# Kernel tuning notes

Measured on AMD Instinct MI355X. Metric: run time of the kernel, lower is better.

The kernel has to match this reference:

```python
import jax, jax.numpy as jnp
import numpy as np

H = 16       # attention heads
DH = 128     # head dim (H*DH = hidden)

def layer_norm(x, scale, bias, eps=1e-5):
    mu = jnp.mean(x, axis=-1, keepdims=True)
    var = jnp.mean(jnp.square(x - mu), axis=-1, keepdims=True)
    return (x - mu) * jax.lax.rsqrt(var + eps) * scale + bias

def transformer_layer(x, ln1_scale, ln1_bias, wq, wk, wv, wo, ln2_scale, ln2_bias, w_ff1, w_ff2):
    B, S, D = x.shape
    xn = layer_norm(x, ln1_scale, ln1_bias)
    q = (xn @ wq.T).reshape(B, S, H, DH)
    k = (xn @ wk.T).reshape(B, S, H, DH)
    v = (xn @ wv.T).reshape(B, S, H, DH)
    scores = jnp.einsum('bqhd,bkhd->bhqk', q, k) / np.sqrt(DH).astype(np.float32)
    causal = jnp.tril(jnp.ones((S, S), dtype=bool))
    scores = jnp.where(causal, scores, jnp.float32(-1e9))
    attn = jax.nn.softmax(scores, axis=-1)
    ctx = jnp.einsum('bhqk,bkhd->bqhd', attn, v).reshape(B, S, D)
    x = x + ctx @ wo.T
    xn2 = layer_norm(x, ln2_scale, ln2_bias)
    x = x + jax.nn.gelu(xn2 @ w_ff1.T) @ w_ff2.T
    return x

def setup_inputs() -> dict:
    key = jax.random.key(0)
    ks = jax.random.split(key, 16)
    B, S, D, R, F = 2, 2048, 2048, 32, 8192
    sd = 1.0 / np.sqrt(D)
    inp = {
        'hidden_states': jax.random.normal(ks[0], (B, S, D), jnp.float32),
        'simple_bias': jnp.zeros((D,), jnp.float32),
        'w_down': jax.random.normal(ks[1], (R, D), jnp.float32) * (0.1 * np.sqrt(2.0 / (D + R))),
        'w_up': jax.random.normal(ks[2], (D, R), jnp.float32) * (0.1 * np.sqrt(2.0 / (D + R))),
        'w_router': jax.random.normal(ks[3], (3, D), jnp.float32) * sd,
        'ln1_scale': jnp.ones((D,), jnp.float32),
        'ln1_bias': jnp.zeros((D,), jnp.float32),
        'wq': jax.random.normal(ks[4], (D, D), jnp.float32) * sd,
        'wk': jax.random.normal(ks[5], (D, D), jnp.float32) * sd,
        'wv': jax.random.normal(ks[6], (D, D), jnp.float32) * sd,
        'wo': jax.random.normal(ks[7], (D, D), jnp.float32) * sd,
        'ln2_scale': jnp.ones((D,), jnp.float32),
        'ln2_bias': jnp.zeros((D,), jnp.float32),
        'w_ff1': jax.random.normal(ks[8], (F, D), jnp.float32) * sd,
        'w_ff2': jax.random.normal(ks[9], (D, F), jnp.float32) * (1.0 / np.sqrt(F)),
    }
    return inp

def reference(hidden_states, simple_bias, w_down, w_up, w_router,
              ln1_scale, ln1_bias, wq, wk, wv, wo,
              ln2_scale, ln2_bias, w_ff1, w_ff2):
    # Router: per-token logits over 3 paths, hard argmax decision
    route_logits = hidden_states @ w_router.T           # [B,S,3]
    route_decisions = jnp.argmax(route_logits, axis=-1)  # [B,S] int
    # Path 0: simple bias add
    out0 = hidden_states + simple_bias
    # Path 1: low-rank residual adapter
    out1 = hidden_states + (hidden_states @ w_down.T) @ w_up.T
    # Path 2: full transformer layer
    out2 = transformer_layer(hidden_states, ln1_scale, ln1_bias, wq, wk, wv, wo,
                             ln2_scale, ln2_bias, w_ff1, w_ff2)
    d = route_decisions[..., None]
    output = jnp.where(d == 0, out0, jnp.where(d == 1, out1, out2))
    return output
```

## Files before the change

### kernel.cpp

```cpp
#include <hip/hip_runtime.h>
#include <math.h>

#define Tn 4096
#define Dn 2048
#define Sn 2048
#define Hn 16
#define Fn 8192
#define Rn 32
#define FC 2048

typedef short bf16x8 __attribute__((ext_vector_type(8)));
typedef float f32x4 __attribute__((ext_vector_type(4)));

union U8 { unsigned short s[8]; uint4 v; };

__device__ __forceinline__ float gelu_f(float x) {
  return 0.5f * x * (1.0f + tanhf(0.7978845608028654f * (x + 0.044715f * x * x * x)));
}

__device__ __forceinline__ unsigned short f2bf(float x) {
  union { float f; unsigned u; } v; v.f = x;
  unsigned r = v.u + 0x7FFFu + ((v.u >> 16) & 1u);
  return (unsigned short)(r >> 16);
}
__device__ __forceinline__ float bf2f(unsigned short h) {
  union { unsigned u; float f; } v; v.u = ((unsigned)h) << 16; return v.f;
}

__device__ __forceinline__ void glds16(const unsigned short* g, unsigned short* lds) {
  __builtin_amdgcn_global_load_lds((const __attribute__((address_space(1))) void*)g,
                                   (__attribute__((address_space(3))) void*)lds, 16, 0, 0);
}

__global__ __launch_bounds__(256)
void ln_router_kernel(const float* __restrict__ x,
                      const float* __restrict__ sc,
                      const float* __restrict__ bi,
                      const float* __restrict__ wr,
                      unsigned short* __restrict__ xh,
                      unsigned short* __restrict__ xl,
                      int* __restrict__ dec)
{
  const int t = blockIdx.x;
  const int tid = threadIdx.x;
  const float* row = x + (size_t)t * Dn;
  const int d0 = tid * 8;
  float4 v0 = *(const float4*)(row + d0);
  float4 v1 = *(const float4*)(row + d0 + 4);
  float a[5];
  a[0] = v0.x + v0.y + v0.z + v0.w + v1.x + v1.y + v1.z + v1.w;
  a[1] = v0.x*v0.x + v0.y*v0.y + v0.z*v0.z + v0.w*v0.w
       + v1.x*v1.x + v1.y*v1.y + v1.z*v1.z + v1.w*v1.w;
  a[2] = 0.f; a[3] = 0.f; a[4] = 0.f;
  if (wr) {
#pragma unroll
    for (int r = 0; r < 3; ++r) {
      float4 w0 = *(const float4*)(wr + r * Dn + d0);
      float4 w1 = *(const float4*)(wr + r * Dn + d0 + 4);
      a[2 + r] = v0.x*w0.x + v0.y*w0.y + v0.z*w0.z + v0.w*w0.w
               + v1.x*w1.x + v1.y*w1.y + v1.z*w1.z + v1.w*w1.w;
    }
  }
#pragma unroll
  for (int i = 0; i < 5; ++i) {
#pragma unroll
    for (int off = 32; off > 0; off >>= 1)
      a[i] += __shfl_down(a[i], off);
  }
  __shared__ float red[4][5];
  __shared__ float fin[5];
  const int wv = tid >> 6, ln = tid & 63;
  if (ln == 0) {
#pragma unroll
    for (int i = 0; i < 5; ++i) red[wv][i] = a[i];
  }
  __syncthreads();
  if (tid == 0) {
#pragma unroll
    for (int i = 0; i < 5; ++i)
      fin[i] = red[0][i] + red[1][i] + red[2][i] + red[3][i];
    if (dec) {
      float l0 = fin[2], l1 = fin[3], l2 = fin[4];
      int best = 0; float bl = l0;
      if (l1 > bl) { best = 1; bl = l1; }
      if (l2 > bl) { best = 2; }
      dec[t] = best;
    }
  }
  __syncthreads();
  const float mu  = fin[0] * (1.0f / Dn);
  const float var = fin[1] * (1.0f / Dn) - mu * mu;
  const float rs  = rsqrtf(var + 1e-5f);
  float4 s0 = *(const float4*)(sc + d0);
  float4 s1 = *(const float4*)(sc + d0 + 4);
  float4 b0 = *(const float4*)(bi + d0);
  float4 b1 = *(const float4*)(bi + d0 + 4);
  float o[8];
  o[0] = (v0.x - mu) * rs * s0.x + b0.x;
  o[1] = (v0.y - mu) * rs * s0.y + b0.y;
  o[2] = (v0.z - mu) * rs * s0.z + b0.z;
  o[3] = (v0.w - mu) * rs * s0.w + b0.w;
  o[4] = (v1.x - mu) * rs * s1.x + b1.x;
  o[5] = (v1.y - mu) * rs * s1.y + b1.y;
  o[6] = (v1.z - mu) * rs * s1.z + b1.z;
  o[7] = (v1.w - mu) * rs * s1.w + b1.w;
  U8 hu, lu;
#pragma unroll
  for (int j = 0; j < 8; ++j) {
    hu.s[j] = f2bf(o[j]);
    lu.s[j] = f2bf(o[j] - bf2f(hu.s[j]));
  }
  *(uint4*)&xh[(size_t)t * Dn + d0] = hu.v;
  *(uint4*)&xl[(size_t)t * Dn + d0] = lu.v;
}

__global__ __launch_bounds__(256)
void cvt_pair_kernel(const float* __restrict__ src, int ld, int K,
                     unsigned short* __restrict__ H, unsigned short* __restrict__ L,
                     int total8)
{
  int i = blockIdx.x * 256 + threadIdx.x;
  if (i >= total8) return;
  size_t e = (size_t)i * 8;
  int row = (int)(e / (size_t)K);
  int col = (int)(e % (size_t)K);
  const float* s = src + (size_t)row * ld + col;
  float4 v0 = *(const float4*)s;
  float4 v1 = *(const float4*)(s + 4);
  float o[8] = {v0.x, v0.y, v0.z, v0.w, v1.x, v1.y, v1.z, v1.w};
  U8 hu, lu;
#pragma unroll
  for (int j = 0; j < 8; ++j) {
    hu.s[j] = f2bf(o[j]);
    lu.s[j] = f2bf(o[j] - bf2f(hu.s[j]));
  }
  *(uint4*)&H[e] = hu.v;
  *(uint4*)&L[e] = lu.v;
}

#define BM 128
#define BN 128
#define BK 32
__global__ __launch_bounds__(256)
void gemm_bf16s(const unsigned short* __restrict__ Ah, const unsigned short* __restrict__ Al,
                const unsigned short* __restrict__ Bh, const unsigned short* __restrict__ Bl,
                int K, float* __restrict__ C, const float* __restrict__ resid,
                unsigned short* __restrict__ Gh, unsigned short* __restrict__ Gl,
                int N, int mode)
{
  __shared__ unsigned short sAh[BM * BK];
  __shared__ unsigned short sAl[BM * BK];
  __shared__ unsigned short sBh[BN * BK];
  __shared__ unsigned short sBl[BN * BK];
  const int tid = threadIdx.x;
  const int l = tid & 63, w = tid >> 6;
  const int wm = w >> 1, wn = w & 1;
  const int fr = l & 15, kg = (l >> 4) * 8;
  const int bm = blockIdx.y * BM, bn = blockIdx.x * BN;

  f32x4 acc[4][4];
#pragma unroll
  for (int m = 0; m < 4; ++m)
#pragma unroll
    for (int n = 0; n < 4; ++n)
#pragma unroll
      for (int q = 0; q < 4; ++q) acc[m][n][q] = 0.f;

  for (int k0 = 0; k0 < K; k0 += BK) {
#pragma unroll
    for (int r = 0; r < 2; ++r) {
      const int c = r * 256 + tid;
      const int row = c >> 2, q = c & 3;
      const size_t ga = (size_t)(bm + row) * K + k0 + q * 8;
      const size_t gb = (size_t)(bn + row) * K + k0 + q * 8;
      const int ub = (r * 256 + w * 64) * 8;
      glds16(Ah + ga, sAh + ub);
      glds16(Al + ga, sAl + ub);
      glds16(Bh + gb, sBh + ub);
      glds16(Bl + gb, sBl + ub);
    }
    __syncthreads();

    bf16x8 ah[4], al[4], bh[4], bl[4];
#pragma unroll
    for (int m = 0; m < 4; ++m) {
      const int ro = (wm * 64 + m * 16 + fr) * BK + kg;
      ah[m] = *(const bf16x8*)&sAh[ro];
      al[m] = *(const bf16x8*)&sAl[ro];
    }
#pragma unroll
    for (int n = 0; n < 4; ++n) {
      const int ro = (wn * 64 + n * 16 + fr) * BK + kg;
      bh[n] = *(const bf16x8*)&sBh[ro];
      bl[n] = *(const bf16x8*)&sBl[ro];
    }
#pragma unroll
    for (int m = 0; m < 4; ++m)
#pragma unroll
      for (int n = 0; n < 4; ++n) {
        acc[m][n] = __builtin_amdgcn_mfma_f32_16x16x32_bf16(ah[m], bh[n], acc[m][n], 0, 0, 0);
        acc[m][n] = __builtin_amdgcn_mfma_f32_16x16x32_bf16(ah[m], bl[n], acc[m][n], 0, 0, 0);
        acc[m][n] = __builtin_amdgcn_mfma_f32_16x16x32_bf16(al[m], bh[n], acc[m][n], 0, 0, 0);
      }
    __syncthreads();
  }

  const int rbase = (l >> 4) * 4;
#pragma unroll
  for (int m = 0; m < 4; ++m) {
#pragma unroll
    for (int i = 0; i < 4; ++i) {
      const int row = bm + wm * 64 + m * 16 + rbase + i;
#pragma unroll
      for (int n = 0; n < 4; ++n) {
        const int col = bn + wn * 64 + n * 16 + fr;
        float v = acc[m][n][i];
        const size_t idx = (size_t)row * N + col;
        if (mode & 5) {
          float g = (mode & 1) ? gelu_f(v) : v;
          unsigned short h = f2bf(g);
          Gh[idx] = h;
          Gl[idx] = f2bf(g - bf2f(h));
        } else {
          if (resid) v += resid[idx];
          if (mode & 2) v += C[idx];
          C[idx] = v;
        }
      }
    }
  }
}

#define GBM 128
#define GBN 128
#define GBK 16
__global__ __launch_bounds__(256)
void gemm_nt(const float* __restrict__ A, int lda,
             const float* __restrict__ B, int ldb,
             float* __restrict__ C, int ldc,
             const float* __restrict__ resid,
             int M, int N, int K, int flags)
{
  __shared__ float As[GBK][GBM + 4];
  __shared__ float Bs[GBK][GBN + 4];
  const int bm = blockIdx.y * GBM;
  const int bn = blockIdx.x * GBN;
  const int tid = threadIdx.x;
  const int ty = tid >> 4, tx = tid & 15;
  float acc[8][8];
#pragma unroll
  for (int i = 0; i < 8; ++i)
#pragma unroll
    for (int j = 0; j < 8; ++j) acc[i][j] = 0.f;

  for (int k0 = 0; k0 < K; k0 += GBK) {
#pragma unroll
    for (int i = 0; i < 2; ++i) {
      int fid = tid + i * 256;
      int row = fid >> 2, c = (fid & 3) << 2;
      float4 av = *(const float4*)(A + (size_t)(bm + row) * lda + k0 + c);
      As[c + 0][row] = av.x; As[c + 1][row] = av.y;
      As[c + 2][row] = av.z; As[c + 3][row] = av.w;
      float4 bv = make_float4(0.f, 0.f, 0.f, 0.f);
      if (bn + row < N)
        bv = *(const float4*)(B + (size_t)(bn + row) * ldb + k0 + c);
      Bs[c + 0][row] = bv.x; Bs[c + 1][row] = bv.y;
      Bs[c + 2][row] = bv.z; Bs[c + 3][row] = bv.w;
    }
    __syncthreads();
#pragma unroll
    for (int k = 0; k < GBK; ++k) {
      float4 a0 = *(const float4*)&As[k][ty * 4];
      float4 a1 = *(const float4*)&As[k][64 + ty * 4];
      float4 b0 = *(const float4*)&Bs[k][tx * 4];
      float4 b1 = *(const float4*)&Bs[k][64 + tx * 4];
      float aa[8] = {a0.x, a0.y, a0.z, a0.w, a1.x, a1.y, a1.z, a1.w};
      float bb[8] = {b0.x, b0.y, b0.z, b0.w, b1.x, b1.y, b1.z, b1.w};
#pragma unroll
      for (int i = 0; i < 8; ++i)
#pragma unroll
        for (int j = 0; j < 8; ++j)
          acc[i][j] += aa[i] * bb[j];
    }
    __syncthreads();
  }
#pragma unroll
  for (int i = 0; i < 8; ++i) {
    int row = bm + ((i < 4) ? (ty * 4 + i) : (64 + ty * 4 + i - 4));
#pragma unroll
    for (int jj = 0; jj < 2; ++jj) {
      int col = bn + ((jj == 0) ? (tx * 4) : (64 + tx * 4));
      if (col < N) {
        float4 o;
        o.x = acc[i][jj * 4 + 0]; o.y = acc[i][jj * 4 + 1];
        o.z = acc[i][jj * 4 + 2]; o.w = acc[i][jj * 4 + 3];
        if (flags & 1) { o.x = gelu_f(o.x); o.y = gelu_f(o.y); o.z = gelu_f(o.z); o.w = gelu_f(o.w); }
        size_t cidx = (size_t)row * ldc + col;
        if (resid) {
          float4 rv = *(const float4*)(resid + cidx);
          o.x += rv.x; o.y += rv.y; o.z += rv.z; o.w += rv.w;
        }
        if (flags & 2) {
          float4 cv = *(const float4*)(C + cidx);
          o.x += cv.x; o.y += cv.y; o.z += cv.z; o.w += cv.w;
        }
        *(float4*)(C + cidx) = o;
      }
    }
  }
}

__global__ __launch_bounds__(256)
void vtrans_kernel(const unsigned short* __restrict__ Vh, const unsigned short* __restrict__ Vl,
                   unsigned short* __restrict__ Th, unsigned short* __restrict__ Tl)
{
  __shared__ unsigned short T[64][68];
  const int j0 = blockIdx.x * 64;
  const int d0 = blockIdx.y * 64;
  const int bh = blockIdx.z;
  const int b = bh >> 4, h = bh & 15;
  const int tid = threadIdx.x;
  const int jr = tid >> 2, cc = (tid & 3) * 16;
  const size_t inrow = ((size_t)b * Sn + j0 + jr) * Dn + h * 128 + d0 + cc;
  const int dr = tid >> 2, jc = (tid & 3) * 16;
  const size_t outrow = ((size_t)bh * 128 + d0 + dr) * (size_t)Sn + j0 + jc;
#pragma unroll
  for (int pass = 0; pass < 2; ++pass) {
    const unsigned short* src = pass ? Vl : Vh;
    unsigned short* dst = pass ? Tl : Th;
    ushort4 u[4];
#pragma unroll
    for (int c = 0; c < 4; ++c) u[c] = *(const ushort4*)&src[inrow + c * 4];
    if (pass) __syncthreads();
#pragma unroll
    for (int c = 0; c < 4; ++c) {
      T[cc + c*4 + 0][jr] = u[c].x;
      T[cc + c*4 + 1][jr] = u[c].y;
      T[cc + c*4 + 2][jr] = u[c].z;
      T[cc + c*4 + 3][jr] = u[c].w;
    }
    __syncthreads();
#pragma unroll
    for (int c = 0; c < 4; ++c)
      *(ushort4*)&dst[outrow + c * 4] = *(const ushort4*)&T[dr][jc + c * 4];
  }
}

__global__ __launch_bounds__(256)
void attn_mfma(const unsigned short* __restrict__ Qh, const unsigned short* __restrict__ Ql,
               const unsigned short* __restrict__ Kh, const unsigned short* __restrict__ Kl,
               const unsigned short* __restrict__ Vth, const unsigned short* __restrict__ Vtl,
               unsigned short* __restrict__ Ch, unsigned short* __restrict__ Cl)
{
  const int bh = blockIdx.y;
  const int b = bh >> 4, h = bh & 15;
  const int q0 = blockIdx.x * 64;
  const int tid = threadIdx.x;
  const int w = tid >> 6, l = tid & 63;
  const int lr = l & 15, lg = l >> 4;
  const int q0w = q0 + w * 16;
  const float scl = 0.08838834764831845f;

  const size_t qrow = ((size_t)b * Sn + q0w + lr) * (size_t)Dn + h * 128;
  bf16x8 qfh[4], qfl[4];
#pragma unroll
  for (int ks = 0; ks < 4; ++ks) {
    qfh[ks] = *(const bf16x8*)&Qh[qrow + ks * 32 + lg * 8];
    qfl[ks] = *(const bf16x8*)&Ql[qrow + ks * 32 + lg * 8];
  }

  f32x4 cacc[8];
#pragma unroll
  for (int dt = 0; dt < 8; ++dt)
#pragma unroll
    for (int i = 0; i < 4; ++i) cacc[dt][i] = 0.f;
  float mrun[4], lrun[4];
#pragma unroll
  for (int i = 0; i < 4; ++i) { mrun[i] = -1e30f; lrun[i] = 0.f; }

  __shared__ unsigned short PhB[4][512];
  __shared__ unsigned short PlB[4][512];
  unsigned short* ph = PhB[w];
  unsigned short* pl = PlB[w];

  const size_t krowbase = (size_t)b * Sn * Dn + h * 128;
  const size_t vtbase = (size_t)bh * 128 * (size_t)Sn;
  const int ntw = (q0w + 15) / 32 + 1;

  for (int t = 0; t < ntw; ++t) {
    const int j0 = t * 32;
    f32x4 s0 = {0.f, 0.f, 0.f, 0.f}, s1 = {0.f, 0.f, 0.f, 0.f};
    const size_t kr0 = krowbase + (size_t)(j0 + lr) * Dn;
    const size_t kr1 = krowbase + (size_t)(j0 + 16 + lr) * Dn;
#pragma unroll
    for (int ks = 0; ks < 4; ++ks) {
      bf16x8 kh0 = *(const bf16x8*)&Kh[kr0 + ks * 32 + lg * 8];
      bf16x8 kl0 = *(const bf16x8*)&Kl[kr0 + ks * 32 + lg * 8];
      s0 = __builtin_amdgcn_mfma_f32_16x16x32_bf16(qfh[ks], kh0, s0, 0, 0, 0);
      s0 = __builtin_amdgcn_mfma_f32_16x16x32_bf16(qfl[ks], kh0, s0, 0, 0, 0);
      s0 = __builtin_amdgcn_mfma_f32_16x16x32_bf16(qfh[ks], kl0, s0, 0, 0, 0);
      bf16x8 kh1 = *(const bf16x8*)&Kh[kr1 + ks * 32 + lg * 8];
      bf16x8 kl1 = *(const bf16x8*)&Kl[kr1 + ks * 32 + lg * 8];
      s1 = __builtin_amdgcn_mfma_f32_16x16x32_bf16(qfh[ks], kh1, s1, 0, 0, 0);
      s1 = __builtin_amdgcn_mfma_f32_16x16x32_bf16(qfl[ks], kh1, s1, 0, 0, 0);
      s1 = __builtin_amdgcn_mfma_f32_16x16x32_bf16(qfh[ks], kl1, s1, 0, 0, 0);
    }
    float p0a[4], p1a[4], cor[4];
#pragma unroll
    for (int i = 0; i < 4; ++i) {
      const int qg = q0w + lg * 4 + i;
      float a0 = s0[i] * scl; if (j0 + lr > qg) a0 = -1e30f;
      float a1 = s1[i] * scl; if (j0 + 16 + lr > qg) a1 = -1e30f;
      float mx = fmaxf(a0, a1);
      mx = fmaxf(mx, __shfl_xor(mx, 1));
      mx = fmaxf(mx, __shfl_xor(mx, 2));
      mx = fmaxf(mx, __shfl_xor(mx, 4));
      mx = fmaxf(mx, __shfl_xor(mx, 8));
      const float mt = fmaxf(mrun[i], mx);
      cor[i] = __expf(mrun[i] - mt);
      mrun[i] = mt;
      float p0 = __expf(a0 - mt);
      float p1 = __expf(a1 - mt);
      p0a[i] = p0; p1a[i] = p1;
      float ls = p0 + p1;
      ls += __shfl_xor(ls, 1);
      ls += __shfl_xor(ls, 2);
      ls += __shfl_xor(ls, 4);
      ls += __shfl_xor(ls, 8);
      lrun[i] = lrun[i] * cor[i] + ls;
    }
#pragma unroll
    for (int i = 0; i < 4; ++i) {
      const int qrl = (lg * 4 + i) * 32;
      unsigned short h0 = f2bf(p0a[i]);
      ph[qrl + lr] = h0;
      pl[qrl + lr] = f2bf(p0a[i] - bf2f(h0));
      unsigned short h1 = f2bf(p1a[i]);
      ph[qrl + 16 + lr] = h1;
      pl[qrl + 16 + lr] = f2bf(p1a[i] - bf2f(h1));
    }
#pragma unroll
    for (int dt = 0; dt < 8; ++dt)
#pragma unroll
      for (int i = 0; i < 4; ++i) cacc[dt][i] *= cor[i];
    bf16x8 pah = *(const bf16x8*)&ph[lr * 32 + lg * 8];
    bf16x8 pal = *(const bf16x8*)&pl[lr * 32 + lg * 8];
#pragma unroll
    for (int dt = 0; dt < 8; ++dt) {
      const size_t vrow = vtbase + (size_t)(dt * 16 + lr) * Sn + j0 + lg * 8;
      bf16x8 vh = *(const bf16x8*)&Vth[vrow];
      bf16x8 vl = *(const bf16x8*)&Vtl[vrow];
      cacc[dt] = __builtin_amdgcn_mfma_f32_16x16x32_bf16(pah, vh, cacc[dt], 0, 0, 0);
      cacc[dt] = __builtin_amdgcn_mfma_f32_16x16x32_bf16(pah, vl, cacc[dt], 0, 0, 0);
      cacc[dt] = __builtin_amdgcn_mfma_f32_16x16x32_bf16(pal, vh, cacc[dt], 0, 0, 0);
    }
  }
#pragma unroll
  for (int i = 0; i < 4; ++i) {
    const float inv = 1.0f / lrun[i];
    const size_t obase = ((size_t)b * Sn + q0w + lg * 4 + i) * Dn + h * 128 + lr;
#pragma unroll
    for (int dt = 0; dt < 8; ++dt) {
      float v = cacc[dt][i] * inv;
      unsigned short hh = f2bf(v);
      Ch[obase + dt * 16] = hh;
      Cl[obase + dt * 16] = f2bf(v - bf2f(hh));
    }
  }
}

__global__ __launch_bounds__(256)
void select_kernel(const float* __restrict__ h, const float* __restrict__ bias,
                   const float* __restrict__ out1,
                   const int* __restrict__ dec, float* __restrict__ out)
{
  int i = blockIdx.x * 256 + threadIdx.x;
  if (i >= Tn * Dn / 4) return;
  int t = i >> 9;
  int de = dec[t];
  if (de == 2) return;
  int d4 = (i & 511) << 2;
  size_t idx = (size_t)t * Dn + d4;
  float4 o;
  if (de == 0) {
    float4 hv = *(const float4*)(h + idx);
    float4 bv = *(const float4*)(bias + d4);
    o.x = hv.x + bv.x; o.y = hv.y + bv.y; o.z = hv.z + bv.z; o.w = hv.w + bv.w;
  } else {
    o = *(const float4*)(out1 + idx);
  }
  *(float4*)(out + idx) = o;
}

extern "C" void kernel_launch(void* const* d_in, const int* in_sizes, int n_in,
                              void* d_out, int out_size, void* d_ws, size_t ws_size,
                              hipStream_t stream) {
  const float* hid    = (const float*)d_in[0];
  const float* sbias  = (const float*)d_in[1];
  const float* w_down = (const float*)d_in[2];
  const float* w_up   = (const float*)d_in[3];
  const float* w_rout = (const float*)d_in[4];
  const float* ln1s   = (const float*)d_in[5];
  const float* ln1b   = (const float*)d_in[6];
  const float* wq     = (const float*)d_in[7];
  const float* wk     = (const float*)d_in[8];
  const float* wv     = (const float*)d_in[9];
  const float* wo     = (const float*)d_in[10];
  const float* ln2s   = (const float*)d_in[11];
  const float* ln2b   = (const float*)d_in[12];
  const float* w_ff1  = (const float*)d_in[13];
  const float* w_ff2  = (const float*)d_in[14];

  const size_t TD  = (size_t)Tn * Dn;
  const size_t WEL = (size_t)Dn * FC;

  char* p = (char*)d_ws;
  auto alloc = [&](size_t bytes) -> char* {
    char* r = p; p += (bytes + 255) & ~(size_t)255; return r;
  };
  unsigned short* P1h = (unsigned short*)alloc(TD * 2);
  unsigned short* P1l = (unsigned short*)alloc(TD * 2);
  unsigned short* B2  = (unsigned short*)alloc(TD * 2);
  unsigned short* B3  = (unsigned short*)alloc(TD * 2);
  unsigned short* B4  = (unsigned short*)alloc(TD * 2);
  unsigned short* B5  = (unsigned short*)alloc(TD * 2);
  unsigned short* B6  = (unsigned short*)alloc(TD * 2);
  unsigned short* B7  = (unsigned short*)alloc(TD * 2);
  unsigned short* Wh  = (unsigned short*)alloc(WEL * 2);
  unsigned short* Wl  = (unsigned short*)alloc(WEL * 2);
  float* hd = (float*)alloc((size_t)Tn * Rn * 4);
  int* dec  = (int*)alloc((size_t)Tn * 4);
  if ((size_t)(p - (char*)d_ws) > ws_size) return;

  unsigned short *Vh = B2, *Vl = B3;
  unsigned short *Qh = B2, *Ql = B3;
  unsigned short *Kh = B4, *Kl = B5;
  unsigned short *Vth = B6, *Vtl = B7;
  float* x2   = (float*)B2;
  unsigned short *Gh = B4, *Gl = B5;
  float* out1 = (float*)B6;
  float* out2 = (float*)d_out;

  const int cw = (int)(WEL / 8 / 256);
  dim3 gq(Dn / BN, Tn / BM);

  ln_router_kernel<<<Tn, 256, 0, stream>>>(hid, ln1s, ln1b, w_rout, P1h, P1l, dec);
  cvt_pair_kernel<<<cw, 256, 0, stream>>>(wv, Dn, Dn, Wh, Wl, (int)(WEL / 8));
  gemm_bf16s<<<gq, 256, 0, stream>>>(P1h, P1l, Wh, Wl, Dn, nullptr, nullptr, Vh, Vl, Dn, 4);
  vtrans_kernel<<<dim3(Sn / 64, 2, 2 * Hn), 256, 0, stream>>>(Vh, Vl, Vth, Vtl);
  cvt_pair_kernel<<<cw, 256, 0, stream>>>(wq, Dn, Dn, Wh, Wl, (int)(WEL / 8));
  gemm_bf16s<<<gq, 256, 0, stream>>>(P1h, P1l, Wh, Wl, Dn, nullptr, nullptr, Qh, Ql, Dn, 4);
  cvt_pair_kernel<<<cw, 256, 0, stream>>>(wk, Dn, Dn, Wh, Wl, (int)(WEL / 8));
  gemm_bf16s<<<gq, 256, 0, stream>>>(P1h, P1l, Wh, Wl, Dn, nullptr, nullptr, Kh, Kl, Dn, 4);
  attn_mfma<<<dim3(Sn / 64, 2 * Hn), 256, 0, stream>>>(Qh, Ql, Kh, Kl, Vth, Vtl, P1h, P1l);
  cvt_pair_kernel<<<cw, 256, 0, stream>>>(wo, Dn, Dn, Wh, Wl, (int)(WEL / 8));
  gemm_bf16s<<<gq, 256, 0, stream>>>(P1h, P1l, Wh, Wl, Dn, x2, hid, nullptr, nullptr, Dn, 0);
  ln_router_kernel<<<Tn, 256, 0, stream>>>(x2, ln2s, ln2b, nullptr, P1h, P1l, nullptr);
  for (int f0 = 0; f0 < Fn; f0 += FC) {
    cvt_pair_kernel<<<cw, 256, 0, stream>>>(w_ff1 + (size_t)f0 * Dn, Dn, Dn, Wh, Wl, (int)(WEL / 8));
    gemm_bf16s<<<gq, 256, 0, stream>>>(P1h, P1l, Wh, Wl, Dn, nullptr, nullptr, Gh, Gl, FC, 1);
    cvt_pair_kernel<<<cw, 256, 0, stream>>>(w_ff2 + f0, Fn, FC, Wh, Wl, (int)(WEL / 8));
    gemm_bf16s<<<gq, 256, 0, stream>>>(Gh, Gl, Wh, Wl, FC, out2,
                                       (f0 == 0) ? x2 : nullptr, nullptr, nullptr, Dn,
                                       (f0 == 0) ? 0 : 2);
  }
  gemm_nt<<<dim3(1, Tn / GBM), 256, 0, stream>>>(hid, Dn, w_down, Dn, hd, Rn, nullptr, Tn, Rn, Dn, 0);
  gemm_nt<<<dim3(Dn / GBN, Tn / GBM), 256, 0, stream>>>(hd, Rn, w_up, Rn, out1, Dn, hid, Tn, Dn, Rn, 0);
  int nv4 = Tn * Dn / 4;
  select_kernel<<<(nv4 + 255) / 256, 256, 0, stream>>>(hid, sbias, out1, dec, (float*)d_out);
}
```

Before: 2.852 ms.

## Compact path-2 tokens so post-attention GEMMs and FFN only process routed rows

A compaction kernel gathers the indices of tokens routed to the full transformer path. The output projection, second layernorm and both FFN GEMMs then work only on those compacted rows, using gathered A-row reads and scattered writes, with early exit for tiles past the count. Attention is also reshaped to single-wave blocks of 16 queries, launched in reverse order so the heavy causal tiles start first. This skips required-by-nobody work for tokens that take the other paths, at the cost of indirect indexing and a device-side count read in every block.

```diff
diff --git a/kernel.cpp b/kernel.cpp
--- a/kernel.cpp
+++ b/kernel.cpp
@@ -39,9 +39,11 @@
                       const float* __restrict__ wr,
                       unsigned short* __restrict__ xh,
                       unsigned short* __restrict__ xl,
-                      int* __restrict__ dec)
+                      int* __restrict__ dec,
+                      const int* __restrict__ mcnt)
 {
   const int t = blockIdx.x;
+  if (mcnt && t >= *mcnt) return;
   const int tid = threadIdx.x;
   const float* row = x + (size_t)t * Dn;
   const int d0 = tid * 8;
@@ -115,6 +117,18 @@
 }
 
 __global__ __launch_bounds__(256)
+void compact_kernel(const int* __restrict__ dec, int* __restrict__ idx2,
+                    int* __restrict__ n2)
+{
+  int t = blockIdx.x * 256 + threadIdx.x;
+  if (t >= Tn) return;
+  if (dec[t] == 2) {
+    int pos = atomicAdd(n2, 1);
+    idx2[pos] = t;
+  }
+}
+
+__global__ __launch_bounds__(256)
 void cvt_pair_kernel(const float* __restrict__ src, int ld, int K,
                      unsigned short* __restrict__ H, unsigned short* __restrict__ L,
                      int total8)
@@ -146,7 +160,9 @@
                 const unsigned short* __restrict__ Bh, const unsigned short* __restrict__ Bl,
                 int K, float* __restrict__ C, const float* __restrict__ resid,
                 unsigned short* __restrict__ Gh, unsigned short* __restrict__ Gl,
-                int N, int mode)
+                int N, int mode,
+                const int* __restrict__ arow, const int* __restrict__ crow,
+                const int* __restrict__ mcnt)
 {
   __shared__ unsigned short sAh[BM * BK];
   __shared__ unsigned short sAl[BM * BK];
@@ -157,6 +173,16 @@
   const int wm = w >> 1, wn = w & 1;
   const int fr = l & 15, kg = (l >> 4) * 8;
   const int bm = blockIdx.y * BM, bn = blockIdx.x * BN;
+  const int M2 = mcnt ? *mcnt : (1 << 30);
+  if (bm >= M2) return;
+
+  int asrc[2];
+#pragma unroll
+  for (int r = 0; r < 2; ++r) {
+    int rr = bm + ((r * 256 + tid) >> 2);
+    if (rr >= M2) rr = M2 - 1;
+    asrc[r] = arow ? arow[rr] : rr;
+  }
 
   f32x4 acc[4][4];
 #pragma unroll
@@ -171,7 +197,7 @@
     for (int r = 0; r < 2; ++r) {
       const int c = r * 256 + tid;
       const int row = c >> 2, q = c & 3;
-      const size_t ga = (size_t)(bm + row) * K + k0 + q * 8;
+      const size_t ga = (size_t)asrc[r] * K + k0 + q * 8;
       const size_t gb = (size_t)(bn + row) * K + k0 + q * 8;
       const int ub = (r * 256 + w * 64) * 8;
       glds16(Ah + ga, sAh + ub);
@@ -210,21 +236,25 @@
   for (int m = 0; m < 4; ++m) {
 #pragma unroll
     for (int i = 0; i < 4; ++i) {
-      const int row = bm + wm * 64 + m * 16 + rbase + i;
+      const int rl = wm * 64 + m * 16 + rbase + i;
+      const int rr = bm + rl;
+      if (rr >= M2) continue;
+      const int cr = crow ? crow[rr] : rr;
+      const int ar = arow ? arow[rr] : rr;
 #pragma unroll
       for (int n = 0; n < 4; ++n) {
         const int col = bn + wn * 64 + n * 16 + fr;
         float v = acc[m][n][i];
-        const size_t idx = (size_t)row * N + col;
+        const size_t idxc = (size_t)cr * N + col;
         if (mode & 5) {
           float g = (mode & 1) ? gelu_f(v) : v;
           unsigned short h = f2bf(g);
-          Gh[idx] = h;
-          Gl[idx] = f2bf(g - bf2f(h));
+          Gh[idxc] = h;
+          Gl[idxc] = f2bf(g - bf2f(h));
         } else {
-          if (resid) v += resid[idx];
-          if (mode & 2) v += C[idx];
-          C[idx] = v;
+          if (resid) v += resid[(size_t)ar * N + col];
+          if (mode & 2) v += C[idxc];
+          C[idxc] = v;
         }
       }
     }
@@ -346,7 +376,7 @@
   }
 }
 
-__global__ __launch_bounds__(256)
+__global__ __launch_bounds__(64, 4)
 void attn_mfma(const unsigned short* __restrict__ Qh, const unsigned short* __restrict__ Ql,
                const unsigned short* __restrict__ Kh, const unsigned short* __restrict__ Kl,
                const unsigned short* __restrict__ Vth, const unsigned short* __restrict__ Vtl,
@@ -354,11 +384,10 @@
 {
   const int bh = blockIdx.y;
   const int b = bh >> 4, h = bh & 15;
-  const int q0 = blockIdx.x * 64;
-  const int tid = threadIdx.x;
-  const int w = tid >> 6, l = tid & 63;
+  const int qt = (gridDim.x - 1) - blockIdx.x;
+  const int q0w = qt * 16;
+  const int l = threadIdx.x & 63;
   const int lr = l & 15, lg = l >> 4;
-  const int q0w = q0 + w * 16;
   const float scl = 0.08838834764831845f;
 
   const size_t qrow = ((size_t)b * Sn + q0w + lr) * (size_t)Dn + h * 128;
@@ -378,10 +407,8 @@
 #pragma unroll
   for (int i = 0; i < 4; ++i) { mrun[i] = -1e30f; lrun[i] = 0.f; }
 
-  __shared__ unsigned short PhB[4][512];
-  __shared__ unsigned short PlB[4][512];
-  unsigned short* ph = PhB[w];
-  unsigned short* pl = PlB[w];
+  __shared__ unsigned short ph[512];
+  __shared__ unsigned short pl[512];
 
   const size_t krowbase = (size_t)b * Sn * Dn + h * 128;
   const size_t vtbase = (size_t)bh * 128 * (size_t)Sn;
@@ -530,13 +557,15 @@
   unsigned short* Wl  = (unsigned short*)alloc(WEL * 2);
   float* hd = (float*)alloc((size_t)Tn * Rn * 4);
   int* dec  = (int*)alloc((size_t)Tn * 4);
+  int* idx2 = (int*)alloc((size_t)Tn * 4);
+  int* n2d  = (int*)alloc(256);
   if ((size_t)(p - (char*)d_ws) > ws_size) return;
 
   unsigned short *Vh = B2, *Vl = B3;
   unsigned short *Qh = B2, *Ql = B3;
   unsigned short *Kh = B4, *Kl = B5;
   unsigned short *Vth = B6, *Vtl = B7;
-  float* x2   = (float*)B2;
+  float* x2c  = (float*)B2;
   unsigned short *Gh = B4, *Gl = B5;
   float* out1 = (float*)B6;
   float* out2 = (float*)d_out;
@@ -544,25 +573,33 @@
   const int cw = (int)(WEL / 8 / 256);
   dim3 gq(Dn / BN, Tn / BM);
 
-  ln_router_kernel<<<Tn, 256, 0, stream>>>(hid, ln1s, ln1b, w_rout, P1h, P1l, dec);
+  ln_router_kernel<<<Tn, 256, 0, stream>>>(hid, ln1s, ln1b, w_rout, P1h, P1l, dec, nullptr);
+  hipMemsetAsync(n2d, 0, sizeof(int), stream);
+  compact_kernel<<<Tn / 256, 256, 0, stream>>>(dec, idx2, n2d);
   cvt_pair_kernel<<<cw, 256, 0, stream>>>(wv, Dn, Dn, Wh, Wl, (int)(WEL / 8));
-  gemm_bf16s<<<gq, 256, 0, stream>>>(P1h, P1l, Wh, Wl, Dn, nullptr, nullptr, Vh, Vl, Dn, 4);
+  gemm_bf16s<<<gq, 256, 0, stream>>>(P1h, P1l, Wh, Wl, Dn, nullptr, nullptr, Vh, Vl, Dn, 4,
+                                     nullptr, nullptr, nullptr);
   vtrans_kernel<<<dim3(Sn / 64, 2, 2 * Hn), 256, 0, stream>>>(Vh, Vl, Vth, Vtl);
   cvt_pair_kernel<<<cw, 256, 0, stream>>>(wq, Dn, Dn, Wh, Wl, (int)(WEL / 8));
-  gemm_bf16s<<<gq, 256, 0, stream>>>(P1h, P1l, Wh, Wl, Dn, nullptr, nullptr, Qh, Ql, Dn, 4);
+  gemm_bf16s<<<gq, 256, 0, stream>>>(P1h, P1l, Wh, Wl, Dn, nullptr, nullptr, Qh, Ql, Dn, 4,
+                                     nullptr, nullptr, nullptr);
   cvt_pair_kernel<<<cw, 256, 0, stream>>>(wk, Dn, Dn, Wh, Wl, (int)(WEL / 8));
-  gemm_bf16s<<<gq, 256, 0, stream>>>(P1h, P1l, Wh, Wl, Dn, nullptr, nullptr, Kh, Kl, Dn, 4);
-  attn_mfma<<<dim3(Sn / 64, 2 * Hn), 256, 0, stream>>>(Qh, Ql, Kh, Kl, Vth, Vtl, P1h, P1l);
+  gemm_bf16s<<<gq, 256, 0, stream>>>(P1h, P1l, Wh, Wl, Dn, nullptr, nullptr, Kh, Kl, Dn, 4,
+                                     nullptr, nullptr, nullptr);
+  attn_mfma<<<dim3(Sn / 16, 2 * Hn), 64, 0, stream>>>(Qh, Ql, Kh, Kl, Vth, Vtl, P1h, P1l);
   cvt_pair_kernel<<<cw, 256, 0, stream>>>(wo, Dn, Dn, Wh, Wl, (int)(WEL / 8));
-  gemm_bf16s<<<gq, 256, 0, stream>>>(P1h, P1l, Wh, Wl, Dn, x2, hid, nullptr, nullptr, Dn, 0);
-  ln_router_kernel<<<Tn, 256, 0, stream>>>(x2, ln2s, ln2b, nullptr, P1h, P1l, nullptr);
+  gemm_bf16s<<<gq, 256, 0, stream>>>(P1h, P1l, Wh, Wl, Dn, x2c, hid, nullptr, nullptr, Dn, 0,
+                                     idx2, nullptr, n2d);
+  ln_router_kernel<<<Tn, 256, 0, stream>>>(x2c, ln2s, ln2b, nullptr, P1h, P1l, nullptr, n2d);
   for (int f0 = 0; f0 < Fn; f0 += FC) {
     cvt_pair_kernel<<<cw, 256, 0, stream>>>(w_ff1 + (size_t)f0 * Dn, Dn, Dn, Wh, Wl, (int)(WEL / 8));
-    gemm_bf16s<<<gq, 256, 0, stream>>>(P1h, P1l, Wh, Wl, Dn, nullptr, nullptr, Gh, Gl, FC, 1);
+    gemm_bf16s<<<gq, 256, 0, stream>>>(P1h, P1l, Wh, Wl, Dn, nullptr, nullptr, Gh, Gl, FC, 1,
+                                       nullptr, nullptr, n2d);
     cvt_pair_kernel<<<cw, 256, 0, stream>>>(w_ff2 + f0, Fn, FC, Wh, Wl, (int)(WEL / 8));
     gemm_bf16s<<<gq, 256, 0, stream>>>(Gh, Gl, Wh, Wl, FC, out2,
-                                       (f0 == 0) ? x2 : nullptr, nullptr, nullptr, Dn,
-                                       (f0 == 0) ? 0 : 2);
+                                       (f0 == 0) ? x2c : nullptr, nullptr, nullptr, Dn,
+                                       (f0 == 0) ? 0 : 2,
+                                       nullptr, idx2, n2d);
   }
   gemm_nt<<<dim3(1, Tn / GBM), 256, 0, stream>>>(hid, Dn, w_down, Dn, hd, Rn, nullptr, Tn, Rn, Dn, 0);
   gemm_nt<<<dim3(Dn / GBN, Tn / GBM), 256, 0, stream>>>(hd, Rn, w_up, Rn, out1, Dn, hid, Tn, Dn, Rn, 0);
```

Result: faster. 2.750 ms (-3.6%).
